# Optimization experiments

Measured on AMD Instinct MI355X. Metric: run time of the kernel, lower is better.

## Reference

```python
import jax, jax.numpy as jnp
import numpy as np
import math

M = 0.2
S = 30.0
COS_M = math.cos(M); SIN_M = math.sin(M)
TH = math.cos(math.pi - M)          # threshold used in torch.where
MM = math.sin(math.pi - M) * M      # linear penalty past threshold
EPS_LS = 0.1                        # CrossEntropyLoss label_smoothing


def _normalize(a, axis=-1):
    return a / jnp.clip(jnp.linalg.norm(a, axis=axis, keepdims=True), 1e-12)


def setup_inputs() -> dict:
    key = jax.random.key(0)
    k1, k2, k3, k4, k5 = jax.random.split(key, 5)
    B, D, C = 2048, 512, 10000
    x = jax.random.normal(k1, (B, D), dtype=jnp.float32)
    label = jax.random.randint(k2, (B,), 0, 1000)  # valid class ids, ~2 per class
    std = math.sqrt(2.0 / (C + D))  # xavier_normal gain=1
    weight = jax.random.normal(k3, (C, D), dtype=jnp.float32) * std    # self.weight (w)
    weight_m = jax.random.normal(k4, (C, D), dtype=jnp.float32) * std  # self.weight_m (wq)
    weight_n = jax.random.uniform(k5, (C, D), dtype=jnp.float32)       # self.weight_n (wk)
    return {"x": x, "label": label, "weight": weight, "weight_m": weight_m, "weight_n": weight_n}


def reference(x, label, weight, weight_m, weight_n):
    B = x.shape[0]
    C = weight.shape[0]
    xn = _normalize(x)                                   # [B, D]

    # ---- AAM (ArcFace) branch ----
    cosine = xn @ _normalize(weight).T                   # [B, C]
    sine = jnp.sqrt(jnp.clip(1.0 - cosine * cosine, 0.0, 1.0))
    phi = cosine * COS_M - sine * SIN_M
    phi = jnp.where(cosine - TH > 0, phi, cosine - MM)
    one_hot = jax.nn.one_hot(label, C, dtype=cosine.dtype)
    output = (one_hot * phi + (1.0 - one_hot) * cosine) * S
    logp = jax.nn.log_softmax(output, axis=-1)
    q_target = one_hot * (1.0 - EPS_LS) + EPS_LS / C     # label smoothing
    aam_loss = -jnp.mean(jnp.sum(q_target * logp, axis=-1))

    # ---- Control-Contrastive branch ----
    label_matrix = label[:, None] == label[None, :]      # [B, B] bool
    q = xn @ _normalize(weight_m[label]).T               # [B, B]
    k = xn @ _normalize(weight_n[label]).T               # [B, B]
    sim = q * k                                          # elementwise, [B, B]

    lm = label_matrix.astype(sim.dtype)
    ap_m = jnp.sum(sim * lm, axis=1) / jnp.sum(lm, axis=1)  # masked row means, [B]
    ap = jnp.diagonal(sim)                                   # [B]
    an = jnp.where(label_matrix, 0.0, sim)                   # [B, B]

    cos_ap = jnp.clip(ap, 0.0, 1.0)
    sin_ap = jnp.sqrt(jnp.clip(1.0 - cos_ap, 0.0, 1.0))
    cos_apm = jnp.clip(ap_m, 0.0, 1.0)
    sin_apm = jnp.sqrt(jnp.clip(1.0 - cos_apm, 0.0, 1.0))
    cos_an = jnp.clip(an, 0.0, 1.0)
    sin_an = jnp.sqrt(jnp.clip(1.0 - cos_an, 0.0, 1.0))

    phi_pm_c = cos_ap * cos_apm - sin_ap * sin_apm       # [B]
    phi_pm_s = jnp.sqrt(jnp.clip(1.0 - phi_pm_c, 0.0, 1.0))
    phi_pm = phi_pm_c * COS_M - phi_pm_s * SIN_M
    logit_neg = 1.0 - phi_pm                              # [B]

    # torch broadcasting [B,B]*[B] -> broadcast over rows (axis 0)
    phi_nm_s = sin_an * cos_apm[None, :] + cos_an * sin_apm[None, :]
    phi_nm_c = jnp.sqrt(jnp.clip(1.0 - phi_nm_s, 0.0, 1.0))
    phi_nm = phi_nm_s * COS_M - phi_nm_c * SIN_M          # [B, B]

    # ragged boolean-indexed logsumexp == masked logsumexp over whole matrix
    lse_n = jax.nn.logsumexp(jnp.where(label_matrix, -jnp.inf, phi_nm))
    lse_neg = jax.nn.logsumexp(logit_neg)
    cc_loss = jax.nn.softplus(lse_n + lse_neg)

    return aam_loss + cc_loss
```

## Files before the change

### kernel.cpp

```cpp
#include <hip/hip_runtime.h>
#include <hip/hip_bf16.h>

typedef unsigned short u16;
typedef unsigned char u8;
typedef unsigned int u32;
typedef _Float16 f16;
typedef _Float16 f16x8 __attribute__((ext_vector_type(8)));
typedef float f32x4 __attribute__((ext_vector_type(4)));
typedef unsigned int u32x4 __attribute__((ext_vector_type(4)));
typedef unsigned int u32x2 __attribute__((ext_vector_type(2)));
typedef long v2i64 __attribute__((ext_vector_type(2)));

constexpr int BATCH = 2048;
constexpr int DIM   = 512;
constexpr int NCLS  = 10000;
constexpr int NPAD  = 10240;

#define F_S     30.0f
#define F_COS_M 0.9800665778412416f
#define F_SIN_M 0.19866933079506122f
#define F_TH   (-0.9800665778412416f)
#define F_MM    0.03973386615901224f

#define G_AAM  1280
#define G_CC    512

static __device__ __forceinline__ float clampf(float v, float lo, float hi) {
    return fminf(fmaxf(v, lo), hi);
}
static __device__ __forceinline__ u32 pk4_fp8(float a, float b, float c, float d) {
    u32 w = __builtin_amdgcn_cvt_pk_fp8_f32(a, b, 0, false);
    w = __builtin_amdgcn_cvt_pk_fp8_f32(c, d, w, true);
    return w;
}
static __device__ __forceinline__ void glds16(const void* g, void* l) {
    __builtin_amdgcn_global_load_lds(
        (const __attribute__((address_space(1))) unsigned int*)g,
        (__attribute__((address_space(3))) unsigned int*)l, 16, 0, 0);
}
static __device__ __forceinline__ float blk_sum(float v, float* sh, int t) {
#pragma unroll
    for (int o = 32; o > 0; o >>= 1) v += __shfl_down(v, o, 64);
    __syncthreads();
    if ((t & 63) == 0) sh[t >> 6] = v;
    __syncthreads();
    return sh[0] + sh[1] + sh[2] + sh[3];
}

__global__ __launch_bounds__(256) void norm_all_kernel(const float* __restrict__ x,
                                                       const float* __restrict__ w,
                                                       const float* __restrict__ wm,
                                                       const float* __restrict__ wn,
                                                       const int* __restrict__ label,
                                                       u8* __restrict__ xnb,
                                                       u8* __restrict__ wb,
                                                       u8* __restrict__ wqb,
                                                       u8* __restrict__ wkb,
                                                       float* __restrict__ zacc) {
    const int t = threadIdx.x, lane = t & 63, wv = t >> 6;
    const int b = blockIdx.x;
    if (b < 33) zacc[b * 256 + t] = 0.f;

    const int row = b * 4 + wv;
    const float* src;
    u8* dst;
    if (row < BATCH) {
        src = x + (size_t)row * DIM;
        dst = xnb + (size_t)row * DIM;
    } else if (row < BATCH + NPAD) {
        const int r = row - BATCH;
        dst = wb + (size_t)r * DIM;
        if (r >= NCLS) {
            u32x2 z = {0, 0};
            *(u32x2*)(dst + lane * 8) = z;
            return;
        }
        src = w + (size_t)r * DIM;
    } else if (row < BATCH + NPAD + BATCH) {
        const int i = row - (BATCH + NPAD);
        src = wm + (size_t)label[i] * DIM;
        dst = wqb + (size_t)i * DIM;
    } else {
        const int i = row - (BATCH + NPAD + BATCH);
        src = wn + (size_t)label[i] * DIM;
        dst = wkb + (size_t)i * DIM;
    }
    const float4 v0 = ((const float4*)src)[lane * 2];
    const float4 v1 = ((const float4*)src)[lane * 2 + 1];
    float s = v0.x * v0.x + v0.y * v0.y + v0.z * v0.z + v0.w * v0.w
            + v1.x * v1.x + v1.y * v1.y + v1.z * v1.z + v1.w * v1.w;
#pragma unroll
    for (int o = 32; o > 0; o >>= 1) s += __shfl_xor(s, o, 64);
    const float inv = 1.0f / fmaxf(sqrtf(s), 1e-12f);
    u32 lo = pk4_fp8(v0.x * inv, v0.y * inv, v0.z * inv, v0.w * inv);
    u32 hi = pk4_fp8(v1.x * inv, v1.y * inv, v1.z * inv, v1.w * inv);
    const int p = 8 * (lane >> 3) + 4 * (lane & 1) + ((lane >> 1) & 3);
    u32x2 o2;
    o2[0] = __shfl(lo, p, 64);
    o2[1] = __shfl(hi, p, 64);
    *(u32x2*)(dst + lane * 8) = o2;
}

__global__ __launch_bounds__(256, 4) void gemm_fused_kernel(const u8* __restrict__ A,
                                                            const u8* __restrict__ Bw,
                                                            const u8* __restrict__ Bq,
                                                            const u8* __restrict__ Bk,
                                                            const int* __restrict__ label,
                                                            float* __restrict__ sumexp,
                                                            float* __restrict__ sumlogit,
                                                            float* __restrict__ philab,
                                                            f16* __restrict__ sim,
                                                            float* __restrict__ msum,
                                                            float* __restrict__ mcnt,
                                                            float* __restrict__ ap) {
    __shared__ __align__(16) u8 sA[2][8192];
    __shared__ __align__(16) u8 sB[2][8192];
    float* red0 = (float*)&sA[0][0];
    float* red1 = (float*)&sA[0][512];

    const int t = threadIdx.x;
    const int lane = t & 63, wave = t >> 6;
    const int fr = lane & 15, quad = lane >> 4;
    const int gl = quad ^ ((fr >> 1) & 3);

    const int srow = t >> 2;
    const int sg   = (t & 3) ^ ((t >> 3) & 3);

    if (blockIdx.x < G_AAM) {
        const int flat = blockIdx.x;
        const int xcd = flat & 7, r = flat >> 3;
        const int bm = r & 15;
        const int bn = (r >> 4) * 8 + xcd;

        const int wm = (wave >> 1) * 64, wn = (wave & 1) * 64;
        const u8* ag = A  + (size_t)(bm * 128 + srow) * DIM + sg * 16;
        const u8* bg = Bw + (size_t)(bn * 128 + srow) * DIM + sg * 16;

        f32x4 acc[4][4] = {};

#define STAGE_AAM(buf, ko)                                              \
        do {                                                            \
            glds16(ag + (ko),            &sA[buf][t * 16]);             \
            glds16(ag + 64 * DIM + (ko), &sA[buf][4096 + t * 16]);      \
            glds16(bg + (ko),            &sB[buf][t * 16]);             \
            glds16(bg + 64 * DIM + (ko), &sB[buf][4096 + t * 16]);      \
        } while (0)

        STAGE_AAM(0, 0);
#pragma unroll
        for (int kb = 0; kb < 8; kb++) {
            const int cur = kb & 1;
            asm volatile("s_waitcnt vmcnt(0)" ::: "memory");
            __builtin_amdgcn_s_barrier();
            asm volatile("" ::: "memory");
            if (kb < 7) STAGE_AAM(cur ^ 1, (kb + 1) * 64);

            const u8* sAc = sA[cur];
            const u8* sBc = sB[cur];
            v2i64 a8[4], b8[4];
#pragma unroll
            for (int f = 0; f < 4; f++) {
                a8[f] = __builtin_bit_cast(v2i64, *(const u32x4*)&sAc[(wm + f * 16 + fr) * 64 + gl * 16]);
                b8[f] = __builtin_bit_cast(v2i64, *(const u32x4*)&sBc[(wn + f * 16 + fr) * 64 + gl * 16]);
            }
            __builtin_amdgcn_s_setprio(1);
#pragma unroll
            for (int i = 0; i < 4; i++)
#pragma unroll
                for (int j = 0; j < 4; j++) {
                    acc[i][j] = __builtin_amdgcn_mfma_f32_16x16x32_fp8_fp8(a8[i][0], b8[j][0], acc[i][j], 0, 0, 0);
                    acc[i][j] = __builtin_amdgcn_mfma_f32_16x16x32_fp8_fp8(a8[i][1], b8[j][1], acc[i][j], 0, 0, 0);
                }
            __builtin_amdgcn_s_setprio(0);
            asm volatile("s_waitcnt lgkmcnt(0)" ::: "memory");
        }
#undef STAGE_AAM

        if (t < 128) { red0[t] = 0.f; red1[t] = 0.f; }
        __syncthreads();

#pragma unroll
        for (int i = 0; i < 4; i++) {
#pragma unroll
            for (int r3 = 0; r3 < 4; r3++) {
                const int ml = wm + i * 16 + quad * 4 + r3;
                const int mg = bm * 128 + ml;
                const int lab = label[mg];
                float esum = 0.f, lsum = 0.f;
#pragma unroll
                for (int j = 0; j < 4; j++) {
                    const int ng = bn * 128 + wn + j * 16 + fr;
                    if (ng < NCLS) {
                        float cv = acc[i][j][r3];
                        float logit;
                        if (ng == lab) {
                            float sine = sqrtf(clampf(1.f - cv * cv, 0.f, 1.f));
                            float phi = cv * F_COS_M - sine * F_SIN_M;
                            float val = ((cv - F_TH) > 0.f) ? phi : (cv - F_MM);
                            logit = F_S * val;
                            philab[mg] = logit;
                        } else {
                            logit = F_S * cv;
                        }
                        esum += __expf(logit);
                        lsum += logit;
                    }
                }
#pragma unroll
                for (int off = 1; off < 16; off <<= 1) {
                    esum += __shfl_xor(esum, off, 64);
                    lsum += __shfl_xor(lsum, off, 64);
                }
                if (fr == 0) {
                    atomicAdd(&red0[ml], esum);
                    atomicAdd(&red1[ml], lsum);
                }
            }
        }
        __syncthreads();
        if (t < 128) {
            atomicAdd(&sumexp[bm * 128 + t], red0[t]);
            atomicAdd(&sumlogit[bm * 128 + t], red1[t]);
        }
    } else {
        const int c = blockIdx.x - G_AAM;
        const int xcd = c & 7, r = c >> 3;
        const int bm = r & 15;
        const int bn = (r >> 4) * 8 + xcd;

        const int wm = (wave >> 1) * 64, wn = (wave & 1) * 32;

        const u8* ag = A  + (size_t)(bm * 128 + srow) * DIM + sg * 16;
        const u8* qg = Bq + (size_t)(bn * 64 + srow) * DIM + sg * 16;
        const u8* kg = Bk + (size_t)(bn * 64 + srow) * DIM + sg * 16;

        f32x4 aq[4][2] = {};
        f32x4 ak[4][2] = {};

#define STAGE_CC(buf, ko)                                               \
        do {                                                            \
            glds16(ag + (ko),            &sA[buf][t * 16]);             \
            glds16(ag + 64 * DIM + (ko), &sA[buf][4096 + t * 16]);      \
            glds16(qg + (ko),            &sB[buf][t * 16]);             \
            glds16(kg + (ko),            &sB[buf][4096 + t * 16]);      \
        } while (0)

        STAGE_CC(0, 0);
#pragma unroll
        for (int kb = 0; kb < 8; kb++) {
            const int cur = kb & 1;
            asm volatile("s_waitcnt vmcnt(0)" ::: "memory");
            __builtin_amdgcn_s_barrier();
            asm volatile("" ::: "memory");
            if (kb < 7) STAGE_CC(cur ^ 1, (kb + 1) * 64);

            const u8* sAc = sA[cur];
            const u8* sBc = sB[cur];
            v2i64 a8[4], q8[2], k8[2];
#pragma unroll
            for (int f = 0; f < 4; f++)
                a8[f] = __builtin_bit_cast(v2i64, *(const u32x4*)&sAc[(wm + f * 16 + fr) * 64 + gl * 16]);
#pragma unroll
            for (int f = 0; f < 2; f++) {
                q8[f] = __builtin_bit_cast(v2i64, *(const u32x4*)&sBc[(wn + f * 16 + fr) * 64 + gl * 16]);
                k8[f] = __builtin_bit_cast(v2i64, *(const u32x4*)&sBc[4096 + (wn + f * 16 + fr) * 64 + gl * 16]);
            }
            __builtin_amdgcn_s_setprio(1);
#pragma unroll
            for (int i = 0; i < 4; i++)
#pragma unroll
                for (int j = 0; j < 2; j++) {
                    aq[i][j] = __builtin_amdgcn_mfma_f32_16x16x32_fp8_fp8(a8[i][0], q8[j][0], aq[i][j], 0, 0, 0);
                    aq[i][j] = __builtin_amdgcn_mfma_f32_16x16x32_fp8_fp8(a8[i][1], q8[j][1], aq[i][j], 0, 0, 0);
                    ak[i][j] = __builtin_amdgcn_mfma_f32_16x16x32_fp8_fp8(a8[i][0], k8[j][0], ak[i][j], 0, 0, 0);
                    ak[i][j] = __builtin_amdgcn_mfma_f32_16x16x32_fp8_fp8(a8[i][1], k8[j][1], ak[i][j], 0, 0, 0);
                }
            __builtin_amdgcn_s_setprio(0);
            asm volatile("s_waitcnt lgkmcnt(0)" ::: "memory");
        }
#undef STAGE_CC

        if (t < 128) { red0[t] = 0.f; red1[t] = 0.f; }
        __syncthreads();

        int lab_n[2];
#pragma unroll
        for (int j = 0; j < 2; j++) lab_n[j] = label[bn * 64 + wn + j * 16 + fr];

#pragma unroll
        for (int i = 0; i < 4; i++) {
#pragma unroll
            for (int r3 = 0; r3 < 4; r3++) {
                const int ml = wm + i * 16 + quad * 4 + r3;
                const int mg = bm * 128 + ml;
                const int lm = label[mg];
                float ms = 0.f, mc = 0.f;
#pragma unroll
                for (int j = 0; j < 2; j++) {
                    const int ng = bn * 64 + wn + j * 16 + fr;
                    float s = aq[i][j][r3] * ak[i][j][r3];
                    sim[(size_t)mg * BATCH + ng] = (f16)s;
                    if (lab_n[j] == lm) { ms += s; mc += 1.f; }
                    if (mg == ng) ap[mg] = s;
                }
#pragma unroll
                for (int off = 1; off < 16; off <<= 1) {
                    ms += __shfl_xor(ms, off, 64);
                    mc += __shfl_xor(mc, off, 64);
                }
                if (fr == 0) {
                    atomicAdd(&red0[ml], ms);
                    atomicAdd(&red1[ml], mc);
                }
            }
        }
        __syncthreads();
        if (t < 128) {
            atomicAdd(&msum[bm * 128 + t], red0[t]);
            atomicAdd(&mcnt[bm * 128 + t], red1[t]);
        }
    }
}

__global__ __launch_bounds__(256) void cc_pass2_kernel(const f16* __restrict__ sim,
                                                       const int* __restrict__ label,
                                                       const float* __restrict__ msum,
                                                       const float* __restrict__ mcnt,
                                                       const float* __restrict__ ap,
                                                       const float* __restrict__ sumexp,
                                                       const float* __restrict__ sumlogit,
                                                       const float* __restrict__ philab,
                                                       float* __restrict__ znP,
                                                       float* __restrict__ znegP,
                                                       float* __restrict__ accAP,
                                                       unsigned* __restrict__ tick,
                                                       float* __restrict__ out) {
    __shared__ float sh[4];
    const int t = threadIdx.x, b = blockIdx.x;
    const int r0 = b * 8;

    const int4 l0 = ((const int4*)label)[t * 2];
    const int4 l1 = ((const int4*)label)[t * 2 + 1];
    const f32x4 ms0 = ((const f32x4*)msum)[t * 2];
    const f32x4 ms1 = ((const f32x4*)msum)[t * 2 + 1];
    const f32x4 mc0 = ((const f32x4*)mcnt)[t * 2];
    const f32x4 mc1 = ((const f32x4*)mcnt)[t * 2 + 1];

    f16x8 v[8];
#pragma unroll
    for (int r = 0; r < 8; r++)
        v[r] = ((const f16x8*)(sim + (size_t)(r0 + r) * BATCH))[t];

    int lj[8];
    float caj[8], saj[8];
#pragma unroll
    for (int e = 0; e < 8; e++) {
        lj[e] = (e < 4) ? ((const int*)&l0)[e] : ((const int*)&l1)[e - 4];
        const float msj = (e < 4) ? ms0[e] : ms1[e - 4];
        const float mcj = (e < 4) ? mc0[e] : mc1[e - 4];
        caj[e] = clampf(msj / mcj, 0.f, 1.f);
        saj[e] = sqrtf(clampf(1.f - caj[e], 0.f, 1.f));
    }

    float acc = 0.f;
#pragma unroll
    for (int r = 0; r < 8; r++) {
        const int li = label[r0 + r];
#pragma unroll
        for (int e = 0; e < 8; e++) {
            if (lj[e] != li) {
                float can = clampf((float)v[r][e], 0.f, 1.f);
                float san = sqrtf(clampf(1.f - can, 0.f, 1.f));
                float pns = san * caj[e] + can * saj[e];
                float pnc = sqrtf(clampf(1.f - pns, 0.f, 1.f));
                acc += __expf(pns * F_COS_M - pnc * F_SIN_M);
            }
        }
    }
    acc = blk_sum(acc, sh, t);

    const int bk = b & 31;
    if (t < 8) {
        const int rr = r0 + t;
        float lse = logf(sumexp[rr]);
        float apart = 0.9f * (philab[rr] - lse) + 1e-5f * (sumlogit[rr] - (float)NCLS * lse);
        float cam = clampf(msum[rr] / mcnt[rr], 0.f, 1.f);
        float sam = sqrtf(clampf(1.f - cam, 0.f, 1.f));
        float cap = clampf(ap[rr], 0.f, 1.f);
        float sap = sqrtf(clampf(1.f - cap, 0.f, 1.f));
        float ppc = cap * cam - sap * sam;
        float pps = sqrtf(clampf(1.f - ppc, 0.f, 1.f));
        float epart = __expf(1.f - (ppc * F_COS_M - pps * F_SIN_M));

        if (t == 0) atomicAdd(&znP[bk], acc);
        atomicAdd(&accAP[bk], apart);
        atomicAdd(&znegP[bk], epart);
    }
    if (t == 0) {
        asm volatile("s_waitcnt vmcnt(0)" ::: "memory");
        unsigned old = __hip_atomic_fetch_add(tick, 1u, __ATOMIC_RELAXED, __HIP_MEMORY_SCOPE_AGENT);
        if (old == 255u) {
            float znv = 0.f, aav = 0.f, zgv = 0.f;
            for (int k = 0; k < 32; k++) {
                znv += __hip_atomic_load(znP + k,   __ATOMIC_RELAXED, __HIP_MEMORY_SCOPE_AGENT);
                aav += __hip_atomic_load(accAP + k, __ATOMIC_RELAXED, __HIP_MEMORY_SCOPE_AGENT);
                zgv += __hip_atomic_load(znegP + k, __ATOMIC_RELAXED, __HIP_MEMORY_SCOPE_AGENT);
            }
            float aam = -aav / (float)BATCH;
            float z = logf(znv) + logf(zgv);
            float cc = (z > 0.f) ? (z + log1pf(__expf(-z))) : log1pf(__expf(z));
            out[0] = aam + cc;
        }
    }
}

extern "C" void kernel_launch(void* const* d_in, const int* in_sizes, int n_in,
                              void* d_out, int out_size, void* d_ws, size_t ws_size,
                              hipStream_t stream) {
    const float* x        = (const float*)d_in[0];
    const int*   label    = (const int*)d_in[1];
    const float* weight   = (const float*)d_in[2];
    const float* weight_m = (const float*)d_in[3];
    const float* weight_n = (const float*)d_in[4];
    float* out = (float*)d_out;
    char* ws = (char*)d_ws;

    const size_t o_xnb  = 0;
    const size_t o_wb   = o_xnb + (size_t)BATCH * DIM;
    const size_t o_wqb  = o_wb  + (size_t)NPAD * DIM;
    const size_t o_wkb  = o_wqb + (size_t)BATCH * DIM;
    const size_t o_sim  = o_wkb + (size_t)BATCH * DIM;
    const size_t o_misc = o_sim + (size_t)BATCH * BATCH * 2;

    u8* xnb = (u8*)(ws + o_xnb);
    u8* wb  = (u8*)(ws + o_wb);
    u8* wqb = (u8*)(ws + o_wqb);
    u8* wkb = (u8*)(ws + o_wkb);
    f16* sim = (f16*)(ws + o_sim);
    float* mf  = (float*)(ws + o_misc);

    float* sumexp   = mf;
    float* sumlogit = mf + 2048;
    float* msum     = mf + 4096;
    float* mcnt     = mf + 6144;
    float* znP      = mf + 8192;
    float* znegP    = mf + 8224;
    float* accAP    = mf + 8256;
    unsigned* tick  = (unsigned*)(mf + 8288);
    float* philab  = mf + 8448;
    float* ap      = mf + 10496;

    norm_all_kernel<<<(BATCH + NPAD + 2 * BATCH) / 4, 256, 0, stream>>>(
        x, weight, weight_m, weight_n, label, xnb, wb, wqb, wkb, mf);

    gemm_fused_kernel<<<G_AAM + G_CC, 256, 0, stream>>>(
        xnb, wb, wqb, wkb, label,
        sumexp, sumlogit, philab, sim, msum, mcnt, ap);

    cc_pass2_kernel<<<256, 256, 0, stream>>>(
        sim, label, msum, mcnt, ap,
        sumexp, sumlogit, philab, znP, znegP, accAP, tick, out);
}
```

Measured before the change: 153.9 us.

## Load GEMM operands directly from global into registers instead of staging through LDS

Removes the LDS double-buffer staging (global_load_lds plus barriers) in both the AAM and contrastive GEMM branches. Each lane now loads its MFMA fragments straight from global memory into a two-stage register buffer and prefetches the next K block. This drops the per-iteration barriers and LDS traffic, but loses data sharing across waves, so each wave re-reads A and B rows from global or L2. It also raises register use, and occupancy is lowered to 3 blocks per SM.

```diff
diff --git a/kernel.cpp b/kernel.cpp
--- a/kernel.cpp
+++ b/kernel.cpp
@@ -32,11 +32,6 @@
     u32 w = __builtin_amdgcn_cvt_pk_fp8_f32(a, b, 0, false);
     w = __builtin_amdgcn_cvt_pk_fp8_f32(c, d, w, true);
     return w;
-}
-static __device__ __forceinline__ void glds16(const void* g, void* l) {
-    __builtin_amdgcn_global_load_lds(
-        (const __attribute__((address_space(1))) unsigned int*)g,
-        (__attribute__((address_space(3))) unsigned int*)l, 16, 0, 0);
 }
 static __device__ __forceinline__ float blk_sum(float v, float* sh, int t) {
 #pragma unroll
@@ -101,7 +96,7 @@
     *(u32x2*)(dst + lane * 8) = o2;
 }
 
-__global__ __launch_bounds__(256, 4) void gemm_fused_kernel(const u8* __restrict__ A,
+__global__ __launch_bounds__(256, 3) void gemm_fused_kernel(const u8* __restrict__ A,
                                                             const u8* __restrict__ Bw,
                                                             const u8* __restrict__ Bq,
                                                             const u8* __restrict__ Bk,
@@ -113,18 +108,14 @@
                                                             float* __restrict__ msum,
                                                             float* __restrict__ mcnt,
                                                             float* __restrict__ ap) {
-    __shared__ __align__(16) u8 sA[2][8192];
-    __shared__ __align__(16) u8 sB[2][8192];
-    float* red0 = (float*)&sA[0][0];
-    float* red1 = (float*)&sA[0][512];
+    __shared__ float red0[128];
+    __shared__ float red1[128];
 
     const int t = threadIdx.x;
     const int lane = t & 63, wave = t >> 6;
     const int fr = lane & 15, quad = lane >> 4;
-    const int gl = quad ^ ((fr >> 1) & 3);
-
-    const int srow = t >> 2;
-    const int sg   = (t & 3) ^ ((t >> 3) & 3);
+
+    if (t < 128) { red0[t] = 0.f; red1[t] = 0.f; }
 
     if (blockIdx.x < G_AAM) {
         const int flat = blockIdx.x;
@@ -133,50 +124,40 @@
         const int bn = (r >> 4) * 8 + xcd;
 
         const int wm = (wave >> 1) * 64, wn = (wave & 1) * 64;
-        const u8* ag = A  + (size_t)(bm * 128 + srow) * DIM + sg * 16;
-        const u8* bg = Bw + (size_t)(bn * 128 + srow) * DIM + sg * 16;
+        const u8* arow = A  + (size_t)(bm * 128 + wm + fr) * DIM + quad * 16;
+        const u8* brow = Bw + (size_t)(bn * 128 + wn + fr) * DIM + quad * 16;
 
         f32x4 acc[4][4] = {};
-
-#define STAGE_AAM(buf, ko)                                              \
-        do {                                                            \
-            glds16(ag + (ko),            &sA[buf][t * 16]);             \
-            glds16(ag + 64 * DIM + (ko), &sA[buf][4096 + t * 16]);      \
-            glds16(bg + (ko),            &sB[buf][t * 16]);             \
-            glds16(bg + 64 * DIM + (ko), &sB[buf][4096 + t * 16]);      \
+        u32x4 a8[2][4], b8[2][4];
+
+#define LOAD_AAM(s, ko)                                                         \
+        do {                                                                    \
+            _Pragma("unroll")                                                   \
+            for (int f = 0; f < 4; f++) {                                       \
+                a8[s][f] = *(const u32x4*)(arow + (size_t)(f * 16) * DIM + (ko)); \
+                b8[s][f] = *(const u32x4*)(brow + (size_t)(f * 16) * DIM + (ko)); \
+            }                                                                   \
         } while (0)
 
-        STAGE_AAM(0, 0);
+        LOAD_AAM(0, 0);
 #pragma unroll
         for (int kb = 0; kb < 8; kb++) {
             const int cur = kb & 1;
-            asm volatile("s_waitcnt vmcnt(0)" ::: "memory");
-            __builtin_amdgcn_s_barrier();
-            asm volatile("" ::: "memory");
-            if (kb < 7) STAGE_AAM(cur ^ 1, (kb + 1) * 64);
-
-            const u8* sAc = sA[cur];
-            const u8* sBc = sB[cur];
-            v2i64 a8[4], b8[4];
-#pragma unroll
-            for (int f = 0; f < 4; f++) {
-                a8[f] = __builtin_bit_cast(v2i64, *(const u32x4*)&sAc[(wm + f * 16 + fr) * 64 + gl * 16]);
-                b8[f] = __builtin_bit_cast(v2i64, *(const u32x4*)&sBc[(wn + f * 16 + fr) * 64 + gl * 16]);
-            }
+            if (kb < 7) LOAD_AAM(cur ^ 1, (kb + 1) * 64);
             __builtin_amdgcn_s_setprio(1);
 #pragma unroll
             for (int i = 0; i < 4; i++)
 #pragma unroll
                 for (int j = 0; j < 4; j++) {
-                    acc[i][j] = __builtin_amdgcn_mfma_f32_16x16x32_fp8_fp8(a8[i][0], b8[j][0], acc[i][j], 0, 0, 0);
-                    acc[i][j] = __builtin_amdgcn_mfma_f32_16x16x32_fp8_fp8(a8[i][1], b8[j][1], acc[i][j], 0, 0, 0);
+                    v2i64 av = __builtin_bit_cast(v2i64, a8[cur][i]);
+                    v2i64 bv = __builtin_bit_cast(v2i64, b8[cur][j]);
+                    acc[i][j] = __builtin_amdgcn_mfma_f32_16x16x32_fp8_fp8(av[0], bv[0], acc[i][j], 0, 0, 0);
+                    acc[i][j] = __builtin_amdgcn_mfma_f32_16x16x32_fp8_fp8(av[1], bv[1], acc[i][j], 0, 0, 0);
                 }
             __builtin_amdgcn_s_setprio(0);
-            asm volatile("s_waitcnt lgkmcnt(0)" ::: "memory");
-        }
-#undef STAGE_AAM
-
-        if (t < 128) { red0[t] = 0.f; red1[t] = 0.f; }
+        }
+#undef LOAD_AAM
+
         __syncthreads();
 
 #pragma unroll
@@ -230,57 +211,48 @@
 
         const int wm = (wave >> 1) * 64, wn = (wave & 1) * 32;
 
-        const u8* ag = A  + (size_t)(bm * 128 + srow) * DIM + sg * 16;
-        const u8* qg = Bq + (size_t)(bn * 64 + srow) * DIM + sg * 16;
-        const u8* kg = Bk + (size_t)(bn * 64 + srow) * DIM + sg * 16;
+        const u8* arow = A  + (size_t)(bm * 128 + wm + fr) * DIM + quad * 16;
+        const u8* qrow = Bq + (size_t)(bn * 64 + wn + fr) * DIM + quad * 16;
+        const u8* krow = Bk + (size_t)(bn * 64 + wn + fr) * DIM + quad * 16;
 
         f32x4 aq[4][2] = {};
         f32x4 ak[4][2] = {};
-
-#define STAGE_CC(buf, ko)                                               \
-        do {                                                            \
-            glds16(ag + (ko),            &sA[buf][t * 16]);             \
-            glds16(ag + 64 * DIM + (ko), &sA[buf][4096 + t * 16]);      \
-            glds16(qg + (ko),            &sB[buf][t * 16]);             \
-            glds16(kg + (ko),            &sB[buf][4096 + t * 16]);      \
+        u32x4 a8[2][4], q8[2][2], k8[2][2];
+
+#define LOAD_CC(s, ko)                                                          \
+        do {                                                                    \
+            _Pragma("unroll")                                                   \
+            for (int f = 0; f < 4; f++)                                         \
+                a8[s][f] = *(const u32x4*)(arow + (size_t)(f * 16) * DIM + (ko)); \
+            _Pragma("unroll")                                                   \
+            for (int f = 0; f < 2; f++) {                                       \
+                q8[s][f] = *(const u32x4*)(qrow + (size_t)(f * 16) * DIM + (ko)); \
+                k8[s][f] = *(const u32x4*)(krow + (size_t)(f * 16) * DIM + (ko)); \
+            }                                                                   \
         } while (0)
 
-        STAGE_CC(0, 0);
+        LOAD_CC(0, 0);
 #pragma unroll
         for (int kb = 0; kb < 8; kb++) {
             const int cur = kb & 1;
-            asm volatile("s_waitcnt vmcnt(0)" ::: "memory");
-            __builtin_amdgcn_s_barrier();
-            asm volatile("" ::: "memory");
-            if (kb < 7) STAGE_CC(cur ^ 1, (kb + 1) * 64);
-
-            const u8* sAc = sA[cur];
-            const u8* sBc = sB[cur];
-            v2i64 a8[4], q8[2], k8[2];
-#pragma unroll
-            for (int f = 0; f < 4; f++)
-                a8[f] = __builtin_bit_cast(v2i64, *(const u32x4*)&sAc[(wm + f * 16 + fr) * 64 + gl * 16]);
-#pragma unroll
-            for (int f = 0; f < 2; f++) {
-                q8[f] = __builtin_bit_cast(v2i64, *(const u32x4*)&sBc[(wn + f * 16 + fr) * 64 + gl * 16]);
-                k8[f] = __builtin_bit_cast(v2i64, *(const u32x4*)&sBc[4096 + (wn + f * 16 + fr) * 64 + gl * 16]);
-            }
+            if (kb < 7) LOAD_CC(cur ^ 1, (kb + 1) * 64);
             __builtin_amdgcn_s_setprio(1);
 #pragma unroll
             for (int i = 0; i < 4; i++)
 #pragma unroll
                 for (int j = 0; j < 2; j++) {
-                    aq[i][j] = __builtin_amdgcn_mfma_f32_16x16x32_fp8_fp8(a8[i][0], q8[j][0], aq[i][j], 0, 0, 0);
-                    aq[i][j] = __builtin_amdgcn_mfma_f32_16x16x32_fp8_fp8(a8[i][1], q8[j][1], aq[i][j], 0, 0, 0);
-                    ak[i][j] = __builtin_amdgcn_mfma_f32_16x16x32_fp8_fp8(a8[i][0], k8[j][0], ak[i][j], 0, 0, 0);
-                    ak[i][j] = __builtin_amdgcn_mfma_f32_16x16x32_fp8_fp8(a8[i][1], k8[j][1], ak[i][j], 0, 0, 0);
+                    v2i64 av = __builtin_bit_cast(v2i64, a8[cur][i]);
+                    v2i64 qv = __builtin_bit_cast(v2i64, q8[cur][j]);
+                    v2i64 kv = __builtin_bit_cast(v2i64, k8[cur][j]);
+                    aq[i][j] = __builtin_amdgcn_mfma_f32_16x16x32_fp8_fp8(av[0], qv[0], aq[i][j], 0, 0, 0);
+                    aq[i][j] = __builtin_amdgcn_mfma_f32_16x16x32_fp8_fp8(av[1], qv[1], aq[i][j], 0, 0, 0);
+                    ak[i][j] = __builtin_amdgcn_mfma_f32_16x16x32_fp8_fp8(av[0], kv[0], ak[i][j], 0, 0, 0);
+                    ak[i][j] = __builtin_amdgcn_mfma_f32_16x16x32_fp8_fp8(av[1], kv[1], ak[i][j], 0, 0, 0);
                 }
             __builtin_amdgcn_s_setprio(0);
-            asm volatile("s_waitcnt lgkmcnt(0)" ::: "memory");
-        }
-#undef STAGE_CC
-
-        if (t < 128) { red0[t] = 0.f; red1[t] = 0.f; }
+        }
+#undef LOAD_CC
+
         __syncthreads();
 
         int lab_n[2];
```

New measurement: 188.1 us. 22.2% more time.
